# Kernel tuning notes

Measured on AMD Instinct MI355X. Metric: run time of the kernel, lower is better.

The kernel has to match this reference:

```python
import jax, jax.numpy as jnp
import numpy as np

B, S, H, I = 2, 2048, 2048, 8192

def setup_inputs() -> dict:
    key = jax.random.key(0)
    k1, k2, k3, k4 = jax.random.split(key, 4)
    x = jax.random.normal(k1, (B, S, H), dtype=jnp.float32)
    gate_w = jax.random.normal(k2, (I, H), dtype=jnp.float32) * 0.02
    up_w = jax.random.normal(k3, (I, H), dtype=jnp.float32) * 0.02
    down_w = jax.random.normal(k4, (H, I), dtype=jnp.float32) * 0.02
    return {"x": x, "gate_w": gate_w, "up_w": up_w, "down_w": down_w}

def reference(x, gate_w, up_w, down_w):
    # SwiGLU FFN forward. In the torch module the hybrid compression only
    # affects activations SAVED for backward; forward output is exact F.linear.
    h_gate = jnp.einsum('bsh,ih->bsi', x, gate_w)   # (B,S,I)
    h_up = jnp.einsum('bsh,ih->bsi', x, up_w)       # (B,S,I)
    h_mid = jax.nn.silu(h_gate) * h_up              # (B,S,I)
    y = jnp.einsum('bsi,hi->bsh', h_mid, down_w)    # (B,S,H)
    return y
```

## Files before the change

kernel.cpp:

```cpp
#include <hip/hip_runtime.h>
#include <hip/hip_bf16.h>
#include <stdint.h>

typedef __attribute__((ext_vector_type(4))) float f32x4;
typedef __attribute__((ext_vector_type(8))) short short8;

__device__ __forceinline__ unsigned short f32_to_bf16_rne(float f) {
  union { float f; unsigned int u; } v; v.f = f;
  unsigned int u = v.u;
  unsigned int r = u + 0x7fffu + ((u >> 16) & 1u);
  return (unsigned short)(r >> 16);
}

#define GLOAD16(gp, lp)                                                 \
  __builtin_amdgcn_global_load_lds(                                     \
      (const __attribute__((address_space(1))) void*)(const void*)(gp), \
      (__attribute__((address_space(3))) void*)(void*)(lp), 16, 0, 0)

#define BAR() __builtin_amdgcn_s_barrier()
#define WAIT_LGKM0() asm volatile("s_waitcnt lgkmcnt(0)" ::: "memory")
#define WAIT_VM8() asm volatile("s_waitcnt vmcnt(8)" ::: "memory")
#define WAIT_VM0() asm volatile("s_waitcnt vmcnt(0)" ::: "memory")

__global__ __launch_bounds__(256) void prep(
    const float* __restrict__ x, const float* __restrict__ g,
    const float* __restrict__ u, const float* __restrict__ dw,
    unsigned short* __restrict__ x_bf, unsigned short* __restrict__ d_bf,
    unsigned short* __restrict__ Bcat, int ldX, int ldD, int ldB) {
  const int NX4 = 2097152;
  const int ND4 = 4194304;
  const int NP4 = 8388608;
  const int total = NX4 + ND4 + NP4;
  int i = blockIdx.x * 256 + threadIdx.x;
  for (; i < total; i += gridDim.x * 256) {
    const float* src;
    unsigned short* dst;
    if (i < NX4) {
      int m = i >> 9, j = i & 511;
      src = x + ((size_t)i << 2);
      dst = x_bf + (size_t)m * ldX + (j << 2);
    } else if (i < NX4 + ND4) {
      int j2 = i - NX4;
      int r_ = j2 >> 11, j = j2 & 2047;
      src = dw + ((size_t)j2 << 2);
      dst = d_bf + (size_t)r_ * ldD + (j << 2);
    } else {
      int j3 = i - NX4 - ND4;
      int R = j3 >> 9, h4 = j3 & 511;
      int grp = R >> 5, s = R & 31;
      src = (s < 16 ? g : u) + (((size_t)(grp * 16 + (s & 15))) << 11) + (h4 << 2);
      dst = Bcat + (size_t)R * ldB + (h4 << 2);
    }
    float4 v = *reinterpret_cast<const float4*>(src);
    ushort4 o;
    o.x = f32_to_bf16_rne(v.x);
    o.y = f32_to_bf16_rne(v.y);
    o.z = f32_to_bf16_rne(v.z);
    o.w = f32_to_bf16_rne(v.w);
    *reinterpret_cast<ushort4*>(dst) = o;
  }
}


#define MFMA_Q(MH, NH)                                                        \
  do {                                                                        \
    _Pragma("unroll") for (int kh = 0; kh < 2; ++kh) {                        \
      _Pragma("unroll") for (int mi = 0; mi < 4; ++mi) {                      \
        _Pragma("unroll") for (int ni = 0; ni < 2; ++ni) {                    \
          acc[(MH)*4 + mi][(NH)*2 + ni] =                                     \
              __builtin_amdgcn_mfma_f32_16x16x32_bf16(                        \
                  a[mi][kh], b[(NH)*2 + ni][kh],                              \
                  acc[(MH)*4 + mi][(NH)*2 + ni], 0, 0, 0);                    \
        }                                                                     \
      }                                                                       \
    }                                                                         \
  } while (0)

#define STAGE(MAT, BUF, H, T)                                                 \
  do {                                                                        \
    const unsigned short* p0_ =                                               \
        MAT##base + (size_t)((H)*128 + r0) * ld##MAT + (size_t)(T)*64 + c0;   \
    const unsigned short* p1_ =                                               \
        MAT##base + (size_t)((H)*128 + r1) * ld##MAT + (size_t)(T)*64 + c1;   \
    GLOAD16(p0_, &s##MAT[BUF][H][off0 >> 1]);                                 \
    GLOAD16(p1_, &s##MAT[BUF][H][(off0 >> 1) + 512]);                         \
  } while (0)

#define LDA(dst, BUF, MI, KH)                                                 \
  {                                                                           \
    int lb_ = ((MI)*16 + frow) * 128 + (KH)*64 + kg * 16;                     \
    int ph_ = lb_ ^ ((frow & 7) << 4);                                        \
    dst = *reinterpret_cast<const short8*>(                                   \
        reinterpret_cast<const char*>(&sA[BUF][wr][0]) + ph_);                \
  }

#define LDB(dst, BUF, NI, KH)                                                 \
  {                                                                           \
    int lb_ = ((wc & 1) * 64 + (NI)*16 + frow) * 128 + (KH)*64 + kg * 16;     \
    int ph_ = lb_ ^ ((frow & 7) << 4);                                        \
    dst = *reinterpret_cast<const short8*>(                                   \
        reinterpret_cast<const char*>(&sB[BUF][wc >> 1][0]) + ph_);           \
  }

template <int EPI>
__global__ __launch_bounds__(512, 2) void gemm8p(
    const unsigned short* __restrict__ A, const unsigned short* __restrict__ B,
    void* __restrict__ Cout, int K, int ldA, int ldB, int ldC,
    int nbm, int nbn) {
  __shared__ unsigned short sA[2][2][128 * 64];
  __shared__ unsigned short sB[2][2][128 * 64];

  const int t = threadIdx.x;
  const int wv = t >> 6, ln = t & 63;
  const int wr = wv >> 2, wc = wv & 3;
  const int frow = ln & 15, kg = ln >> 4;

  const int r = blockIdx.x;
  const int swz = (r & 7) * (gridDim.x >> 3) + (r >> 3);
  const int bm = swz % nbm;
  const int rest = swz / nbm;
  const int bn = rest % nbn;
  const int bz = rest / nbn;

  A += (size_t)bz * K;
  B += (size_t)bz * K;

  const int off0 = wv * 2048 + ln * 16;
  const int off1 = off0 + 1024;
  const int s0 = off0 ^ (((off0 >> 7) & 7) << 4);
  const int s1 = off1 ^ (((off1 >> 7) & 7) << 4);
  const int r0 = s0 >> 7, c0 = (s0 & 127) >> 1;
  const int r1 = s1 >> 7, c1 = (s1 & 127) >> 1;

  const unsigned short* Abase = A + (size_t)(bm * 256) * ldA;
  const unsigned short* Bbase = B + (size_t)(bn * 256) * ldB;

  f32x4 acc[8][4] = {};
  short8 a[4][2], b[4][2];

  const int NT = K >> 6;

  STAGE(A, 0, 0, 0); STAGE(A, 0, 1, 0);
  STAGE(B, 0, 0, 0); STAGE(B, 0, 1, 0);
  STAGE(A, 1, 0, 1); STAGE(A, 1, 1, 1);
  STAGE(B, 1, 0, 1); STAGE(B, 1, 1, 1);
  WAIT_VM8();
  BAR();

  for (int tt = 0; tt < NT; ++tt) {
    const int buf = tt & 1;
#pragma unroll
    for (int mi = 0; mi < 4; ++mi) { LDA(a[mi][0], buf, mi, 0); LDA(a[mi][1], buf, mi, 1); }
#pragma unroll
    for (int ni = 0; ni < 2; ++ni) { LDB(b[ni][0], buf, ni, 0); LDB(b[ni][1], buf, ni, 1); }
    BAR(); WAIT_LGKM0();
    __builtin_amdgcn_s_setprio(1); MFMA_Q(0, 0); __builtin_amdgcn_s_setprio(0);
    BAR();
#pragma unroll
    for (int ni = 2; ni < 4; ++ni) { LDB(b[ni][0], buf, ni, 0); LDB(b[ni][1], buf, ni, 1); }
    BAR(); WAIT_LGKM0();
    __builtin_amdgcn_s_setprio(1); MFMA_Q(0, 1); __builtin_amdgcn_s_setprio(0);
    BAR();
#pragma unroll
    for (int mi = 0; mi < 4; ++mi) { LDA(a[mi][0], buf, mi + 4, 0); LDA(a[mi][1], buf, mi + 4, 1); }
    if (tt + 2 < NT) { STAGE(B, buf, 0, tt + 2); STAGE(B, buf, 1, tt + 2); }
    BAR(); WAIT_LGKM0();
    __builtin_amdgcn_s_setprio(1); MFMA_Q(1, 0); __builtin_amdgcn_s_setprio(0);
    BAR();
    if (tt + 2 < NT) { STAGE(A, buf, 0, tt + 2); STAGE(A, buf, 1, tt + 2); }
    BAR(); WAIT_LGKM0();
    __builtin_amdgcn_s_setprio(1); MFMA_Q(1, 1); __builtin_amdgcn_s_setprio(0);
    if (tt < NT - 1) {
      if (tt + 2 < NT) { WAIT_VM8(); } else { WAIT_VM0(); }
    }
    BAR();
  }

  if (EPI == 0) {
    float* C = reinterpret_cast<float*>(Cout);
    const int rb = bm * 256 + wr * 128 + kg * 4;
    const int cb = bn * 256 + wc * 64 + frow;
#pragma unroll
    for (int mi = 0; mi < 8; ++mi)
#pragma unroll
      for (int ni = 0; ni < 4; ++ni)
#pragma unroll
        for (int j = 0; j < 4; ++j)
          atomicAdd(&C[(size_t)(rb + mi * 16 + j) * ldC + (cb + ni * 16)],
                    acc[mi][ni][j]);
  } else {
    unsigned short* Hm = reinterpret_cast<unsigned short*>(Cout);
    const int rb = bm * 256 + wr * 128 + kg * 4;
    const int cb = bn * 128 + wc * 32 + frow;
#pragma unroll
    for (int mi = 0; mi < 8; ++mi)
#pragma unroll
      for (int p = 0; p < 2; ++p)
#pragma unroll
        for (int j = 0; j < 4; ++j) {
          float gg = acc[mi][2 * p][j];
          float uu = acc[mi][2 * p + 1][j];
          float h = gg * uu * __builtin_amdgcn_rcpf(1.0f + __expf(-gg));
          Hm[(size_t)(rb + mi * 16 + j) * ldC + (cb + p * 16)] = f32_to_bf16_rne(h);
        }
  }
}


extern "C" void kernel_launch(void* const* d_in, const int* in_sizes, int n_in,
                              void* d_out, int out_size, void* d_ws, size_t ws_size,
                              hipStream_t stream) {
  const float* x      = (const float*)d_in[0];
  const float* gate_w = (const float*)d_in[1];
  const float* up_w   = (const float*)d_in[2];
  const float* down_w = (const float*)d_in[3];
  float* y = (float*)d_out;

  const int Mtok = 4096, H = 2048, I = 8192;

  const int PAD = 32;
  size_t need = ((size_t)Mtok * (H + PAD) + (size_t)(2 * I) * (H + PAD) +
                 (size_t)H * (I + PAD) + (size_t)Mtok * (I + PAD)) * 2;
  const int pad = (ws_size >= need) ? PAD : 0;
  const int ldX = H + pad;
  const int ldB = H + pad;
  const int ldD = I + pad;
  const int ldH = I + pad;

  unsigned short* x_bf = (unsigned short*)d_ws;
  unsigned short* Bcat = x_bf + (size_t)Mtok * ldX;
  unsigned short* d_bf = Bcat + (size_t)2 * I * ldB;
  unsigned short* h_bf = d_bf + (size_t)H * ldD;

  hipMemsetAsync(y, 0, (size_t)Mtok * H * sizeof(float), stream);

  prep<<<2048, 256, 0, stream>>>(x, gate_w, up_w, down_w, x_bf, d_bf, Bcat,
                                 ldX, ldD, ldB);

  gemm8p<1><<<dim3(1024), 512, 0, stream>>>(
      x_bf, Bcat, h_bf, H, ldX, ldB, ldH, Mtok / 256, (2 * I) / 256);

  gemm8p<0><<<dim3(256), 512, 0, stream>>>(
      h_bf, d_bf, y, I / 2, ldH, ldD, H, Mtok / 256, H / 256);
}
```

Measured before the change: 529.4 us.

## Replace atomic split-K reduction with bf16 partials and separate reduce kernel

The second GEMM's split-K halves now write bf16 partial outputs into a reused workspace region, and a new kernel sums them into the fp32 output. This removes the memset and the fp32 atomicAdds. The row padding on the workspace buffers is dropped, and the first GEMM gets a bn-major block ordering for better L2 reuse of weight tiles. The cost is an extra launch plus the partial traffic, and rounding the partials to bf16 loses precision in the output, while unpadded rows may bring back LDS or channel conflicts.

```diff
diff --git a/kernel.cpp b/kernel.cpp
--- a/kernel.cpp
+++ b/kernel.cpp
@@ -12,6 +12,12 @@
   return (unsigned short)(r >> 16);
 }
 
+__device__ __forceinline__ float bf16_to_f32(unsigned short h) {
+  union { unsigned int u; float f; } v;
+  v.u = ((unsigned int)h) << 16;
+  return v.f;
+}
+
 #define GLOAD16(gp, lp)                                                 \
   __builtin_amdgcn_global_load_lds(                                     \
       (const __attribute__((address_space(1))) void*)(const void*)(gp), \
@@ -26,7 +32,7 @@
     const float* __restrict__ x, const float* __restrict__ g,
     const float* __restrict__ u, const float* __restrict__ dw,
     unsigned short* __restrict__ x_bf, unsigned short* __restrict__ d_bf,
-    unsigned short* __restrict__ Bcat, int ldX, int ldD, int ldB) {
+    unsigned short* __restrict__ Bcat) {
   const int NX4 = 2097152;
   const int ND4 = 4194304;
   const int NP4 = 8388608;
@@ -36,20 +42,18 @@
     const float* src;
     unsigned short* dst;
     if (i < NX4) {
-      int m = i >> 9, j = i & 511;
       src = x + ((size_t)i << 2);
-      dst = x_bf + (size_t)m * ldX + (j << 2);
+      dst = x_bf + ((size_t)i << 2);
     } else if (i < NX4 + ND4) {
-      int j2 = i - NX4;
-      int r_ = j2 >> 11, j = j2 & 2047;
-      src = dw + ((size_t)j2 << 2);
-      dst = d_bf + (size_t)r_ * ldD + (j << 2);
+      int j = i - NX4;
+      src = dw + ((size_t)j << 2);
+      dst = d_bf + ((size_t)j << 2);
     } else {
-      int j3 = i - NX4 - ND4;
-      int R = j3 >> 9, h4 = j3 & 511;
+      int j = i - NX4 - ND4;
+      int R = j >> 9, h4 = j & 511;
       int grp = R >> 5, s = R & 31;
       src = (s < 16 ? g : u) + (((size_t)(grp * 16 + (s & 15))) << 11) + (h4 << 2);
-      dst = Bcat + (size_t)R * ldB + (h4 << 2);
+      dst = Bcat + ((size_t)j << 2);
     }
     float4 v = *reinterpret_cast<const float4*>(src);
     ushort4 o;
@@ -58,6 +62,24 @@
     o.z = f32_to_bf16_rne(v.z);
     o.w = f32_to_bf16_rne(v.w);
     *reinterpret_cast<ushort4*>(dst) = o;
+  }
+}
+
+__global__ __launch_bounds__(256) void reduce_add_bf16(
+    const unsigned short* __restrict__ a, const unsigned short* __restrict__ b,
+    float* __restrict__ o, int n8) {
+  int i = blockIdx.x * 256 + threadIdx.x;
+  for (; i < n8; i += gridDim.x * 256) {
+    short8 va = reinterpret_cast<const short8*>(a)[i];
+    short8 vb = reinterpret_cast<const short8*>(b)[i];
+    float r[8];
+#pragma unroll
+    for (int j = 0; j < 8; ++j)
+      r[j] = bf16_to_f32((unsigned short)va[j]) + bf16_to_f32((unsigned short)vb[j]);
+    float4 o0 = {r[0], r[1], r[2], r[3]};
+    float4 o1 = {r[4], r[5], r[6], r[7]};
+    reinterpret_cast<float4*>(o)[2 * i] = o0;
+    reinterpret_cast<float4*>(o)[2 * i + 1] = o1;
   }
 }
 
@@ -105,8 +127,8 @@
 template <int EPI>
 __global__ __launch_bounds__(512, 2) void gemm8p(
     const unsigned short* __restrict__ A, const unsigned short* __restrict__ B,
-    void* __restrict__ Cout, int K, int ldA, int ldB, int ldC,
-    int nbm, int nbn) {
+    void* __restrict__ Cout, int K, int ldA, int ldB, int ldC, size_t zstride,
+    int nbm, int nbn, int bnmajor) {
   __shared__ unsigned short sA[2][2][128 * 64];
   __shared__ unsigned short sB[2][2][128 * 64];
 
@@ -116,11 +138,19 @@
   const int frow = ln & 15, kg = ln >> 4;
 
   const int r = blockIdx.x;
-  const int swz = (r & 7) * (gridDim.x >> 3) + (r >> 3);
-  const int bm = swz % nbm;
-  const int rest = swz / nbm;
-  const int bn = rest % nbn;
-  const int bz = rest / nbn;
+  int bm, bn, bz;
+  if (bnmajor) {
+    const int x = r & 7, lin = r >> 3;
+    bn = x * 8 + (lin & 7);
+    bm = lin >> 3;
+    bz = 0;
+  } else {
+    const int swz = (r & 7) * (gridDim.x >> 3) + (r >> 3);
+    bm = swz % nbm;
+    const int rest = swz / nbm;
+    bn = rest % nbn;
+    bz = rest / nbn;
+  }
 
   A += (size_t)bz * K;
   B += (size_t)bz * K;
@@ -177,7 +207,7 @@
   }
 
   if (EPI == 0) {
-    float* C = reinterpret_cast<float*>(Cout);
+    unsigned short* P = reinterpret_cast<unsigned short*>(Cout) + (size_t)bz * zstride;
     const int rb = bm * 256 + wr * 128 + kg * 4;
     const int cb = bn * 256 + wc * 64 + frow;
 #pragma unroll
@@ -186,8 +216,8 @@
       for (int ni = 0; ni < 4; ++ni)
 #pragma unroll
         for (int j = 0; j < 4; ++j)
-          atomicAdd(&C[(size_t)(rb + mi * 16 + j) * ldC + (cb + ni * 16)],
-                    acc[mi][ni][j]);
+          P[(size_t)(rb + mi * 16 + j) * ldC + (cb + ni * 16)] =
+              f32_to_bf16_rne(acc[mi][ni][j]);
   } else {
     unsigned short* Hm = reinterpret_cast<unsigned short*>(Cout);
     const int rb = bm * 256 + wr * 128 + kg * 4;
@@ -218,28 +248,20 @@
 
   const int Mtok = 4096, H = 2048, I = 8192;
 
-  const int PAD = 32;
-  size_t need = ((size_t)Mtok * (H + PAD) + (size_t)(2 * I) * (H + PAD) +
-                 (size_t)H * (I + PAD) + (size_t)Mtok * (I + PAD)) * 2;
-  const int pad = (ws_size >= need) ? PAD : 0;
-  const int ldX = H + pad;
-  const int ldB = H + pad;
-  const int ldD = I + pad;
-  const int ldH = I + pad;
-
   unsigned short* x_bf = (unsigned short*)d_ws;
-  unsigned short* Bcat = x_bf + (size_t)Mtok * ldX;
-  unsigned short* d_bf = Bcat + (size_t)2 * I * ldB;
-  unsigned short* h_bf = d_bf + (size_t)H * ldD;
-
-  hipMemsetAsync(y, 0, (size_t)Mtok * H * sizeof(float), stream);
-
-  prep<<<2048, 256, 0, stream>>>(x, gate_w, up_w, down_w, x_bf, d_bf, Bcat,
-                                 ldX, ldD, ldB);
+  unsigned short* Bcat = x_bf + (size_t)Mtok * H;
+  unsigned short* d_bf = Bcat + (size_t)2 * I * H;
+  unsigned short* h_bf = d_bf + (size_t)H * I;
+  unsigned short* part = Bcat;
+
+  prep<<<2048, 256, 0, stream>>>(x, gate_w, up_w, down_w, x_bf, d_bf, Bcat);
 
   gemm8p<1><<<dim3(1024), 512, 0, stream>>>(
-      x_bf, Bcat, h_bf, H, ldX, ldB, ldH, Mtok / 256, (2 * I) / 256);
+      x_bf, Bcat, h_bf, H, H, H, I, 0, Mtok / 256, (2 * I) / 256, 1);
 
   gemm8p<0><<<dim3(256), 512, 0, stream>>>(
-      h_bf, d_bf, y, I / 2, ldH, ldD, H, Mtok / 256, H / 256);
-}
+      h_bf, d_bf, part, I / 2, I, I, H, (size_t)Mtok * H, Mtok / 256, H / 256, 0);
+
+  reduce_add_bf16<<<2048, 256, 0, stream>>>(part, part + (size_t)Mtok * H, y,
+                                            (Mtok * H) / 8);
+}
```

New measurement: 481.6 us. 1.1x faster.
